# Performance work log

Measured on AMD Instinct MI355X. Metric: run time of the kernel, lower is better.

The kernel has to match this reference:

```python
import jax, jax.numpy as jnp
import numpy as np
from jax import lax

EPS = 1e-5
N_WIRES, N_LAYERS = 4, 3
DIM = 2 ** N_WIRES  # 16

# Static CNOT permutations for control w, target w+1 (state @ CNOT => new[k] = old[k ^ (((k>>c)&1)<<t)])
_idx = np.arange(DIM)
CNOT_PERMS = [jnp.asarray(_idx ^ (((_idx >> w) & 1) << (w + 1))) for w in range(N_WIRES - 1)]


def conv3x3(x, w):
    # x: [B,1,H,W], w: [1,1,3,3], padding=1, no bias
    return lax.conv_general_dilated(x, w, (1, 1), 'SAME',
                                    dimension_numbers=('NCHW', 'OIHW', 'NCHW'))


def batchnorm_train(x, gamma, beta):
    # training-mode BN: batch statistics over (B,H,W), biased variance
    mean = jnp.mean(x, axis=(0, 2, 3), keepdims=True)
    var = jnp.var(x, axis=(0, 2, 3), keepdims=True)
    xn = (x - mean) * lax.rsqrt(var + EPS)
    return xn * gamma.reshape(1, -1, 1, 1) + beta.reshape(1, -1, 1, 1)


def residual_block(x, w1, g1, b1, w2, g2, b2):
    out = jax.nn.relu(batchnorm_train(conv3x3(x, w1), g1, b1))
    out = batchnorm_train(conv3x3(out, w2), g2, b2)
    return jax.nn.relu(out + x)


def quantum_feat4(theta):
    # Faithful to QuantumKernel: real state, each RZ scales by cos(theta/2)
    # (rz[0,0]==rz[1,1]==cos(theta/2)), CNOT is a bit-indexed permutation.
    # State is independent of the patch values (patch is never used).
    s = jnp.zeros(DIM, dtype=theta.dtype).at[0].set(1.0)
    for l in range(N_LAYERS):
        s = s * jnp.prod(jnp.cos(theta[l] / 2.0))  # 8 RZ scalings for this layer
        for w in range(N_WIRES - 1):
            s = s[CNOT_PERMS[w]]
    probs = s ** 2
    return probs[:4]


def setup_inputs() -> dict:
    key = jax.random.key(0)
    ks = jax.random.split(key, 12)
    B = 16384
    d = dict(
        x=jax.random.normal(ks[0], (B, 1, 28, 28), dtype=jnp.float32),
        theta=jax.random.normal(ks[1], (N_LAYERS, N_WIRES, 2), dtype=jnp.float32),
        r1_w1=jax.random.normal(ks[2], (1, 1, 3, 3), dtype=jnp.float32) * 0.3,
        r1_g1=jnp.ones((1,), jnp.float32), r1_b1=jnp.zeros((1,), jnp.float32),
        r1_w2=jax.random.normal(ks[3], (1, 1, 3, 3), dtype=jnp.float32) * 0.3,
        r1_g2=jnp.ones((1,), jnp.float32), r1_b2=jnp.zeros((1,), jnp.float32),
        r2_w1=jax.random.normal(ks[4], (1, 1, 3, 3), dtype=jnp.float32) * 0.3,
        r2_g1=jnp.ones((1,), jnp.float32), r2_b1=jnp.zeros((1,), jnp.float32),
        r2_w2=jax.random.normal(ks[5], (1, 1, 3, 3), dtype=jnp.float32) * 0.3,
        r2_g2=jnp.ones((1,), jnp.float32), r2_b2=jnp.zeros((1,), jnp.float32),
        fc_w=jax.random.normal(ks[6], (10, 784), dtype=jnp.float32) * 0.03,
        fc_b=jnp.zeros((10,), jnp.float32),
        alpha=jnp.asarray(0.5, dtype=jnp.float32),
    )
    return d


def reference(x, theta, r1_w1, r1_g1, r1_b1, r1_w2, r1_g2, r1_b2,
              r2_w1, r2_g1, r2_b1, r2_w2, r2_g2, r2_b2, fc_w, fc_b, alpha):
    B = x.shape[0]
    cls_feat = residual_block(x, r1_w1, r1_g1, r1_b1, r1_w2, r1_g2, r1_b2)
    cls_feat = residual_block(cls_feat, r2_w1, r2_g1, r2_b1, r2_w2, r2_g2, r2_b2)
    cls_flat = cls_feat.reshape(B, -1)  # [B, 784]

    # Quantum filter: kernel output ignores patch values, identical for all
    # 196 patches and all batch elements; cat along dim=1 -> tile the 4-vector.
    p4 = quantum_feat4(theta)                           # [4]
    q_feat = jnp.broadcast_to(jnp.tile(p4, 14 * 14), (B, 784))

    fused = alpha * cls_flat + (1.0 - alpha) * q_feat
    logits = fused @ fc_w.T + fc_b
    return jax.nn.log_softmax(logits, axis=-1)
```

## Files before the change

### kernel.cpp

```cpp
#include <hip/hip_runtime.h>
#include <hip/hip_fp16.h>
#include <math.h>

#define BATCH   16384
#define IMGPIX  784
#define NTOT    (BATCH * IMGPIX)
#define NSLOT   64
#define SLOTSTR 8
#define STAGE_DBL (NSLOT * SLOTSTR)
#define TROW 224
#define TGRP 6272
#define CONVBLK 3584

typedef _Float16 half8 __attribute__((ext_vector_type(8)));
typedef float f32x4 __attribute__((ext_vector_type(4)));

struct __align__(8) h4 { __half2 lo, hi; };
__device__ __forceinline__ h4 f4_to_h4(float4 v) {
    h4 r; r.lo = __floats2half2_rn(v.x, v.y); r.hi = __floats2half2_rn(v.z, v.w); return r;
}
__device__ __forceinline__ float4 h4_to_f4(h4 p) {
    float2 a = __half22float2(p.lo), b = __half22float2(p.hi);
    return make_float4(a.x, a.y, b.x, b.y);
}
#define ZERO4 make_float4(0.f, 0.f, 0.f, 0.f)

__device__ __forceinline__ void block_stats_atomic(double lsum, double lsq, double* slot) {
    __shared__ double red[4][2];
    #pragma unroll
    for (int off = 32; off >= 1; off >>= 1) {
        lsum += __shfl_down(lsum, off, 64);
        lsq  += __shfl_down(lsq,  off, 64);
    }
    const int lane = threadIdx.x & 63;
    const int w    = threadIdx.x >> 6;
    if (lane == 0) { red[w][0] = lsum; red[w][1] = lsq; }
    __syncthreads();
    if (threadIdx.x == 0) {
        double ts = (red[0][0] + red[1][0]) + (red[2][0] + red[3][0]);
        double tq = (red[0][1] + red[1][1]) + (red[2][1] + red[3][1]);
        atomicAdd(&slot[0], ts);
        atomicAdd(&slot[1], tq);
    }
}

__device__ __forceinline__ float2 stats_ab(const double* __restrict__ stats_in,
                                           float gamma, float beta) {
    int lane = threadIdx.x & 63;
    double s = stats_in[lane * SLOTSTR];
    double q = stats_in[lane * SLOTSTR + 1];
    #pragma unroll
    for (int off = 32; off >= 1; off >>= 1) {
        s += __shfl_down(s, off, 64);
        q += __shfl_down(q, off, 64);
    }
    s = __shfl(s, 0, 64);
    q = __shfl(q, 0, 64);
    const double INV_N = 1.0 / (double)NTOT;
    double mean = s * INV_N;
    double var  = q * INV_N - mean * mean;
    float rstd = 1.0f / sqrtf((float)var + 1e-5f);
    float a  = gamma * rstd;
    float bb = beta - (float)mean * a;
    return make_float2(a, bb);
}

__device__ __forceinline__ float4 hrow(float wl, float wc, float wr,
                                       float L, float4 v, float R) {
    float4 h;
    h.x = fmaf(wl, L,   fmaf(wc, v.x, wr * v.y));
    h.y = fmaf(wl, v.x, fmaf(wc, v.y, wr * v.z));
    h.z = fmaf(wl, v.y, fmaf(wc, v.z, wr * v.w));
    h.w = fmaf(wl, v.z, fmaf(wc, v.w, wr * R));
    return h;
}

__device__ __forceinline__ void emit_row(__half* dst, int r, float4 o, float mf,
                                         double& lsum, double& lsq, bool act) {
    if (act) *(h4*)(dst + r * TROW) = f4_to_h4(o);
    float s4 = (o.x + o.y) + (o.z + o.w);
    float q4 = fmaf(o.x, o.x, fmaf(o.y, o.y, fmaf(o.z, o.z, o.w * o.w)));
    lsum += (double)(mf * s4);
    lsq  += (double)(mf * q4);
}

#define LANE_SETUP()                                                          \
    const int t = threadIdx.x;                                                \
    const int lane = t & 63;                                                  \
    const int widx = t >> 6;                                                  \
    const int c4   = lane & 7;                                                \
    const bool act = (c4 < 7);                                                \
    const float mf = act ? 1.f : 0.f;                                         \
    const int c4c  = c4 < 7 ? c4 : 6;                                         \
    const int task = blockIdx.x * 4 + widx;                     \
    const int s    = task >> 11;                              \
    const int G    = task & 2047;                          \
    const int r0   = s * 4;                                                   \
    const int rtop = (r0 > 0)  ? (r0 - 1) : 0;                                \
    const int rbot = (r0 < 24) ? (r0 + 4) : 27;                               \
    const int i8   = lane >> 3;                                               \
    const int img  = G * 8 + i8;                                              \
    const size_t xbase = (size_t)img * IMGPIX + c4c * 4;                      \
    const size_t tbR   = (size_t)G * TGRP + c4c * 32 + i8 * 4;                \
    const size_t tbW   = (size_t)G * TGRP + c4  * 32 + i8 * 4;

#define CONV_STEP(k, v)                                                       \
    {                                                                         \
        float L = __shfl_up((v).w, 1, 64);  if (c4 == 0) L = 0.f;             \
        float R = __shfl_down((v).x, 1, 64); if (c4 == 6) R = 0.f;            \
        float4 h2 = hrow(w9[6], w9[7], w9[8], L, (v), R);                     \
        float4 h1 = hrow(w9[3], w9[4], w9[5], L, (v), R);                     \
        float4 h0 = hrow(w9[0], w9[1], w9[2], L, (v), R);                     \
        accA.x += h2.x; accA.y += h2.y; accA.z += h2.z; accA.w += h2.w;       \
        if ((k) >= 2) emit_row(dst, r0 + (k) - 2, accA, mf, lsum, lsq, act);  \
        accA.x = accB.x + h1.x; accA.y = accB.y + h1.y;                       \
        accA.z = accB.z + h1.z; accA.w = accB.w + h1.w;                       \
        accB = h0;                                                            \
    }

#define HALO_ZERO(k, v)                                                       \
    if ((k) == 0 && r0 == 0)  (v) = ZERO4;                                    \
    if ((k) == 5 && r0 == 24) (v) = ZERO4;

__global__ __launch_bounds__(256, 8) void k_conv_plain(const float* __restrict__ in,
        const float* __restrict__ w, __half* __restrict__ out,
        __half* __restrict__ x16_out, double* __restrict__ stats_out,
        const float* __restrict__ fc_w, const float* __restrict__ fc_b,
        const float* __restrict__ theta, const float* __restrict__ alpha_p,
        __half* __restrict__ Bpack, float* __restrict__ qkpad)
{
    LANE_SETUP();
    float w9[9];
    #pragma unroll
    for (int i = 0; i < 9; i++) w9[i] = w[i];
    const float* src = in + xbase;
    __half* dst  = out + tbW;
    __half* dstx = x16_out + tbW;

    float4 vb[6];
    vb[0] = *(const float4*)(src + rtop * 28);
    #pragma unroll
    for (int k = 1; k < 5; k++) vb[k] = *(const float4*)(src + (r0 - 1 + k) * 28);
    vb[5] = *(const float4*)(src + rbot * 28);
    __builtin_amdgcn_sched_barrier(0);

    float4 accA = ZERO4, accB = ZERO4;
    double lsum = 0.0, lsq = 0.0;
    #pragma unroll
    for (int k = 0; k < 6; k++) {
        float4 v = vb[k];
        if (act && k >= 1 && k <= 4)
            *(h4*)(dstx + (r0 - 1 + k) * TROW) = f4_to_h4(vb[k]);
        HALO_ZERO(k, v);
        CONV_STEP(k, v);
    }
    block_stats_atomic(lsum, lsq, &stats_out[(blockIdx.x & (NSLOT - 1)) * SLOTSTR]);

    if (blockIdx.x < 56) {
        const int idx = blockIdx.x * 256 + t;
        const int r = idx >> 9;
        const int l = (idx >> 3) & 63;
        const int j = idx & 7;
        const int n = l & 15;
        const int c = ((l >> 4) << 3) + j;
        float v = 0.f;
        if (c < 28 && n < 10) v = fc_w[n * 784 + r * 28 + c];
        Bpack[idx] = __float2half(v);
    } else if (blockIdx.x == 56) {
        __shared__ float csum[10];
        if (t < 80) {
            int k = t >> 3, oct = t & 7;
            float sm = 0.f;
            #pragma unroll
            for (int i = 0; i < 25; i++) {
                int p = oct + 8 * i;
                if (p < 196) sm += fc_w[k * 784 + p * 4];
            }
            sm += __shfl_xor(sm, 1, 64);
            sm += __shfl_xor(sm, 2, 64);
            sm += __shfl_xor(sm, 4, 64);
            if (oct == 0) csum[k] = sm;
        }
        __syncthreads();
        if (t < 16) {
            float val = -1e30f;
            if (t < 10) {
                float c = 1.f;
                #pragma unroll
                for (int i = 0; i < 24; i++) c *= cosf(theta[i] * 0.5f);
                val = fmaf((1.f - alpha_p[0]) * c * c, csum[t], fc_b[t]);
            }
            qkpad[t] = val;
        }
    }
}

__global__ __launch_bounds__(256, 8) void k_conv_affine(const __half* __restrict__ in,
        const double* __restrict__ stats_in,
        const float* __restrict__ gamma, const float* __restrict__ beta,
        const float* __restrict__ w, __half* __restrict__ out, double* __restrict__ stats_out)
{
    LANE_SETUP();
    float2 ab = stats_ab(stats_in, gamma[0], beta[0]);
    float w9[9];
    #pragma unroll
    for (int i = 0; i < 9; i++) w9[i] = w[i];
    const __half* src = in + tbR;
    __half* dst = out + tbW;

    h4 vb[6];
    vb[0] = *(const h4*)(src + rtop * TROW);
    #pragma unroll
    for (int k = 1; k < 5; k++) vb[k] = *(const h4*)(src + (r0 - 1 + k) * TROW);
    vb[5] = *(const h4*)(src + rbot * TROW);
    __builtin_amdgcn_sched_barrier(0);

    float4 accA = ZERO4, accB = ZERO4;
    double lsum = 0.0, lsq = 0.0;
    #pragma unroll
    for (int k = 0; k < 6; k++) {
        float4 r4 = h4_to_f4(vb[k]);
        float4 v;
        v.x = fmaxf(fmaf(ab.x, r4.x, ab.y), 0.f);
        v.y = fmaxf(fmaf(ab.x, r4.y, ab.y), 0.f);
        v.z = fmaxf(fmaf(ab.x, r4.z, ab.y), 0.f);
        v.w = fmaxf(fmaf(ab.x, r4.w, ab.y), 0.f);
        HALO_ZERO(k, v);
        CONV_STEP(k, v);
    }
    block_stats_atomic(lsum, lsq, &stats_out[(blockIdx.x & (NSLOT - 1)) * SLOTSTR]);
}

__global__ __launch_bounds__(256, 8) void k_conv_resid(const __half* __restrict__ y2,
        const __half* __restrict__ x16, const double* __restrict__ stats_in,
        const float* __restrict__ gamma, const float* __restrict__ beta,
        const float* __restrict__ w, __half* __restrict__ y3_out,
        __half* __restrict__ o1_out, double* __restrict__ stats_out)
{
    LANE_SETUP();
    float2 ab = stats_ab(stats_in, gamma[0], beta[0]);
    float w9[9];
    #pragma unroll
    for (int i = 0; i < 9; i++) w9[i] = w[i];
    const __half* srcy = y2 + tbR;
    const __half* srcx = x16 + tbR;
    __half* dst  = y3_out + tbW;
    __half* dsto = o1_out + tbW;

    h4 yb[6], xb[6];
    yb[0] = *(const h4*)(srcy + rtop * TROW);
    xb[0] = *(const h4*)(srcx + rtop * TROW);
    #pragma unroll
    for (int k = 1; k < 5; k++) {
        yb[k] = *(const h4*)(srcy + (r0 - 1 + k) * TROW);
        xb[k] = *(const h4*)(srcx + (r0 - 1 + k) * TROW);
    }
    yb[5] = *(const h4*)(srcy + rbot * TROW);
    xb[5] = *(const h4*)(srcx + rbot * TROW);
    __builtin_amdgcn_sched_barrier(0);

    float4 accA = ZERO4, accB = ZERO4;
    double lsum = 0.0, lsq = 0.0;
    #pragma unroll
    for (int k = 0; k < 6; k++) {
        float4 r4 = h4_to_f4(yb[k]);
        float4 x4 = h4_to_f4(xb[k]);
        float4 v;
        v.x = fmaxf(fmaf(ab.x, r4.x, ab.y) + x4.x, 0.f);
        v.y = fmaxf(fmaf(ab.x, r4.y, ab.y) + x4.y, 0.f);
        v.z = fmaxf(fmaf(ab.x, r4.z, ab.y) + x4.z, 0.f);
        v.w = fmaxf(fmaf(ab.x, r4.w, ab.y) + x4.w, 0.f);
        HALO_ZERO(k, v);
        if (act && k >= 1 && k <= 4)
            *(h4*)(dsto + (r0 - 1 + k) * TROW) = f4_to_h4(v);
        CONV_STEP(k, v);
    }
    block_stats_atomic(lsum, lsq, &stats_out[(blockIdx.x & (NSLOT - 1)) * SLOTSTR]);
}

__global__ __launch_bounds__(256, 4) void k_head_mfma(const __half* __restrict__ y4,
        const __half* __restrict__ o1, const double* __restrict__ stats_in,
        const float* __restrict__ gamma, const float* __restrict__ beta,
        const __half* __restrict__ Bpack, const float* __restrict__ qkpad,
        const float* __restrict__ alpha_p, float* __restrict__ out)
{
    __shared__ float accs[4][64][4];
    const int t    = threadIdx.x;
    const int lane = t & 63;
    const int q    = t >> 6;
    float2 ab = stats_ab(stats_in, gamma[0], beta[0]);

    const int m   = lane & 15;
    const int jg  = lane >> 4;
    const int c4a = jg * 2;
    const int c4b = (jg == 3) ? 6 : (jg * 2 + 1);
    const int G   = blockIdx.x * 2 + (m >> 3);
    const int i8  = m & 7;
    const size_t base = (size_t)G * TGRP + i8 * 4;
    const __half* ya = y4 + base;
    const __half* oa = o1 + base;

    f32x4 acc = {0.f, 0.f, 0.f, 0.f};
    #pragma unroll
    for (int rr = 0; rr < 7; rr++) {
        const int r  = q * 7 + rr;
        const int ro = r * TROW;
        h4 ylo = *(const h4*)(ya + ro + c4a * 32);
        h4 yhi = *(const h4*)(ya + ro + c4b * 32);
        h4 olo = *(const h4*)(oa + ro + c4a * 32);
        h4 ohi = *(const h4*)(oa + ro + c4b * 32);
        float4 yf0 = h4_to_f4(ylo), yf1 = h4_to_f4(yhi);
        float4 of0 = h4_to_f4(olo), of1 = h4_to_f4(ohi);
        float4 va, vb;
        va.x = fmaxf(fmaf(ab.x, yf0.x, ab.y) + of0.x, 0.f);
        va.y = fmaxf(fmaf(ab.x, yf0.y, ab.y) + of0.y, 0.f);
        va.z = fmaxf(fmaf(ab.x, yf0.z, ab.y) + of0.z, 0.f);
        va.w = fmaxf(fmaf(ab.x, yf0.w, ab.y) + of0.w, 0.f);
        vb.x = fmaxf(fmaf(ab.x, yf1.x, ab.y) + of1.x, 0.f);
        vb.y = fmaxf(fmaf(ab.x, yf1.y, ab.y) + of1.y, 0.f);
        vb.z = fmaxf(fmaf(ab.x, yf1.z, ab.y) + of1.z, 0.f);
        vb.w = fmaxf(fmaf(ab.x, yf1.w, ab.y) + of1.w, 0.f);
        union { half8 v; h4 qq[2]; } A;
        A.qq[0] = f4_to_h4(va);
        A.qq[1] = f4_to_h4(vb);
        half8 B = *(const half8*)(Bpack + (r * 64 + lane) * 8);
        acc = __builtin_amdgcn_mfma_f32_16x16x32_f16(A.v, B, acc, 0, 0, 0);
    }
    #pragma unroll
    for (int i = 0; i < 4; i++) accs[q][lane][i] = acc[i];
    __syncthreads();

    if (t < 64) {
        float c[4];
        #pragma unroll
        for (int i = 0; i < 4; i++)
            c[i] = (accs[0][lane][i] + accs[1][lane][i])
                 + (accs[2][lane][i] + accs[3][lane][i]);
        const float alpha = alpha_p[0];
        const int cls = lane & 15;
        const float qv = qkpad[cls];
        #pragma unroll
        for (int i = 0; i < 4; i++) {
            float logit = fmaf(alpha, c[i], qv);
            float mx = logit;
            mx = fmaxf(mx, __shfl_xor(mx, 1, 64));
            mx = fmaxf(mx, __shfl_xor(mx, 2, 64));
            mx = fmaxf(mx, __shfl_xor(mx, 4, 64));
            mx = fmaxf(mx, __shfl_xor(mx, 8, 64));
            float se = __expf(logit - mx);
            se += __shfl_xor(se, 1, 64);
            se += __shfl_xor(se, 2, 64);
            se += __shfl_xor(se, 4, 64);
            se += __shfl_xor(se, 8, 64);
            float lse = mx + __logf(se);
            if (cls < 10) {
                int img = blockIdx.x * 16 + (lane >> 4) * 4 + i;
                out[(size_t)img * 10 + cls] = logit - lse;
            }
        }
    }
}

extern "C" void kernel_launch(void* const* d_in, const int* in_sizes, int n_in,
                              void* d_out, int out_size, void* d_ws, size_t ws_size,
                              hipStream_t stream) {
    const float* x     = (const float*)d_in[0];
    const float* theta = (const float*)d_in[1];
    const float* r1_w1 = (const float*)d_in[2];
    const float* r1_g1 = (const float*)d_in[3];
    const float* r1_b1 = (const float*)d_in[4];
    const float* r1_w2 = (const float*)d_in[5];
    const float* r1_g2 = (const float*)d_in[6];
    const float* r1_b2 = (const float*)d_in[7];
    const float* r2_w1 = (const float*)d_in[8];
    const float* r2_g1 = (const float*)d_in[9];
    const float* r2_b1 = (const float*)d_in[10];
    const float* r2_w2 = (const float*)d_in[11];
    const float* r2_g2 = (const float*)d_in[12];
    const float* r2_b2 = (const float*)d_in[13];
    const float* fc_w  = (const float*)d_in[14];
    const float* fc_b  = (const float*)d_in[15];
    const float* alpha = (const float*)d_in[16];
    float* out = (float*)d_out;

    double* stats = (double*)d_ws;
    float*  qkpad = (float*)((char*)d_ws + 16384);
    __half* Bpack = (__half*)((char*)d_ws + 16448);
    __half* bufA  = (__half*)((char*)d_ws + 65536);
    __half* bufB  = bufA + (size_t)NTOT;
    __half* bufD  = bufB + (size_t)NTOT;
    __half* bufX  = bufD + (size_t)NTOT;

    double* s_y1 = stats + 0 * STAGE_DBL;
    double* s_y2 = stats + 1 * STAGE_DBL;
    double* s_y3 = stats + 2 * STAGE_DBL;
    double* s_y4 = stats + 3 * STAGE_DBL;

    hipMemsetAsync(stats, 0, 4 * STAGE_DBL * sizeof(double), stream);
    k_conv_plain<<<CONVBLK, 256, 0, stream>>>(x, r1_w1, bufA, bufX, s_y1,
                                              fc_w, fc_b, theta, alpha,
                                              Bpack, qkpad);
    k_conv_affine<<<CONVBLK, 256, 0, stream>>>(bufA, s_y1, r1_g1, r1_b1, r1_w2, bufB, s_y2);
    k_conv_resid<<<CONVBLK, 256, 0, stream>>>(bufB, bufX, s_y2, r1_g2, r1_b2, r2_w1, bufA, bufD, s_y3);
    k_conv_affine<<<CONVBLK, 256, 0, stream>>>(bufA, s_y3, r2_g1, r2_b1, r2_w2, bufB, s_y4);
    k_head_mfma<<<1024, 256, 0, stream>>>(bufB, bufD, s_y4, r2_g2, r2_b2,
                                          Bpack, qkpad, alpha, out);
}
```

Measured before the change: 89.95 us.

## Stage first conv input group through LDS with coalesced loads and writes

The first conv kernel now assigns one block per 8-image group. It loads the fp32 input with fully coalesced float4 reads, converts it to half and transposes it into the tiled LDS layout, then writes the half copy out contiguously. Each wave convolves 7 rows from LDS instead of gathering strided rows from global memory with halo re-reads. This cuts redundant halo loads and scattered accesses, at the cost of 12.5KB of LDS per block, an extra barrier and fewer blocks (2048). The side tasks that depend on blockIdx.x < 57 still run because the grid remains large enough.

New measurement: 90.73 us. Within noise of the previous version (+0.9%).

```diff
diff --git a/kernel.cpp b/kernel.cpp
--- a/kernel.cpp
+++ b/kernel.cpp
@@ -99,8 +99,6 @@
     const int rtop = (r0 > 0)  ? (r0 - 1) : 0;                                \
     const int rbot = (r0 < 24) ? (r0 + 4) : 27;                               \
     const int i8   = lane >> 3;                                               \
-    const int img  = G * 8 + i8;                                              \
-    const size_t xbase = (size_t)img * IMGPIX + c4c * 4;                      \
     const size_t tbR   = (size_t)G * TGRP + c4c * 32 + i8 * 4;                \
     const size_t tbW   = (size_t)G * TGRP + c4  * 32 + i8 * 4;
 
@@ -129,29 +127,46 @@
         const float* __restrict__ theta, const float* __restrict__ alpha_p,
         __half* __restrict__ Bpack, float* __restrict__ qkpad)
 {
-    LANE_SETUP();
+    __shared__ __half xs[28 * TROW];
+    const int t    = threadIdx.x;
+    const int lane = t & 63;
+    const int q    = t >> 6;
+    const int G    = blockIdx.x;
     float w9[9];
     #pragma unroll
     for (int i = 0; i < 9; i++) w9[i] = w[i];
-    const float* src = in + xbase;
-    __half* dst  = out + tbW;
-    __half* dstx = x16_out + tbW;
-
-    float4 vb[6];
-    vb[0] = *(const float4*)(src + rtop * 28);
-    #pragma unroll
-    for (int k = 1; k < 5; k++) vb[k] = *(const float4*)(src + (r0 - 1 + k) * 28);
-    vb[5] = *(const float4*)(src + rbot * 28);
-    __builtin_amdgcn_sched_barrier(0);
+
+    const float4* xg = (const float4*)(in + (size_t)G * 8 * IMGPIX);
+    for (int f = t; f < 1568; f += 256) {
+        float4 v = xg[f];
+        int il = f / 196;
+        int p  = f - il * 196;
+        int r  = p / 7;
+        int c4s = p - r * 7;
+        *(h4*)(&xs[r * TROW + c4s * 32 + il * 4]) = f4_to_h4(v);
+    }
+    __syncthreads();
+
+    __half* xo = x16_out + (size_t)G * TGRP;
+    for (int f = t; f < 1568; f += 256)
+        *(h4*)(xo + f * 4) = *(const h4*)(&xs[f * 4]);
+
+    const int c4   = lane & 7;
+    const bool act = (c4 < 7);
+    const float mf = act ? 1.f : 0.f;
+    const int c4c  = c4 < 7 ? c4 : 6;
+    const int i8   = lane >> 3;
+    const int r0   = q * 7;
+    __half* dst = out + (size_t)G * TGRP + c4 * 32 + i8 * 4;
 
     float4 accA = ZERO4, accB = ZERO4;
     double lsum = 0.0, lsq = 0.0;
     #pragma unroll
-    for (int k = 0; k < 6; k++) {
-        float4 v = vb[k];
-        if (act && k >= 1 && k <= 4)
-            *(h4*)(dstx + (r0 - 1 + k) * TROW) = f4_to_h4(vb[k]);
-        HALO_ZERO(k, v);
+    for (int k = 0; k < 9; k++) {
+        const int rr = r0 - 1 + k;
+        const int rc = rr < 0 ? 0 : (rr > 27 ? 27 : rr);
+        float4 v = h4_to_f4(*(const h4*)(&xs[rc * TROW + c4c * 32 + i8 * 4]));
+        if (rr < 0 || rr > 27) v = ZERO4;
         CONV_STEP(k, v);
     }
     block_stats_atomic(lsum, lsq, &stats_out[(blockIdx.x & (NSLOT - 1)) * SLOTSTR]);
@@ -397,9 +412,9 @@
     double* s_y4 = stats + 3 * STAGE_DBL;
 
     hipMemsetAsync(stats, 0, 4 * STAGE_DBL * sizeof(double), stream);
-    k_conv_plain<<<CONVBLK, 256, 0, stream>>>(x, r1_w1, bufA, bufX, s_y1,
-                                              fc_w, fc_b, theta, alpha,
-                                              Bpack, qkpad);
+    k_conv_plain<<<2048, 256, 0, stream>>>(x, r1_w1, bufA, bufX, s_y1,
+                                           fc_w, fc_b, theta, alpha,
+                                           Bpack, qkpad);
     k_conv_affine<<<CONVBLK, 256, 0, stream>>>(bufA, s_y1, r1_g1, r1_b1, r1_w2, bufB, s_y2);
     k_conv_resid<<<CONVBLK, 256, 0, stream>>>(bufB, bufX, s_y2, r1_g2, r1_b2, r2_w1, bufA, bufD, s_y3);
     k_conv_affine<<<CONVBLK, 256, 0, stream>>>(bufA, s_y3, r2_g1, r2_b1, r2_w2, bufB, s_y4);
```
